# Kernel tuning notes

Hardware: AMD Instinct MI355X
Metric: run time of the kernel (lower is better)

Reference implementation:

```python
import jax, jax.numpy as jnp
import numpy as np

N_NODES = 50000
N_EDGES = 800000
D_FEAT = 128
HIDDEN = 128
BERT_DIM = 768
BATCH = 4096
MAX_ENT = 20
COMB = BERT_DIM + HIDDEN  # 896


def setup_inputs() -> dict:
    key = jax.random.key(0)
    ks = jax.random.split(key, 12)
    article_bert_embeddings = jax.random.normal(ks[0], (BATCH, BERT_DIM), dtype=jnp.float32)
    x = jax.random.normal(ks[1], (N_NODES, D_FEAT), dtype=jnp.float32)
    edge_index = jax.random.randint(ks[2], (2, N_EDGES), 0, N_NODES, dtype=jnp.int64)
    entity_map = jax.random.randint(ks[3], (BATCH, MAX_ENT), 0, N_NODES, dtype=jnp.int64)
    pad = jax.random.uniform(ks[4], (BATCH, MAX_ENT)) < 0.3
    entity_map = jnp.where(pad, jnp.int64(-1), entity_map)
    s = 1.0 / np.sqrt(D_FEAT)
    W1 = jax.random.normal(ks[5], (D_FEAT, HIDDEN), dtype=jnp.float32) * s
    b1 = jnp.zeros((HIDDEN,), dtype=jnp.float32)
    W2 = jax.random.normal(ks[6], (HIDDEN, HIDDEN), dtype=jnp.float32) * (1.0 / np.sqrt(HIDDEN))
    b2 = jnp.zeros((HIDDEN,), dtype=jnp.float32)
    fc1_w = jax.random.normal(ks[7], (COMB, COMB // 2), dtype=jnp.float32) * (1.0 / np.sqrt(COMB))
    fc1_b = jnp.zeros((COMB // 2,), dtype=jnp.float32)
    fc2_w = jax.random.normal(ks[8], (COMB // 2, 1), dtype=jnp.float32) * (1.0 / np.sqrt(COMB // 2))
    fc2_b = jnp.zeros((1,), dtype=jnp.float32)
    return dict(article_bert_embeddings=article_bert_embeddings, x=x,
                edge_index=edge_index, entity_map=entity_map,
                W1=W1, b1=b1, W2=W2, b2=b2,
                fc1_w=fc1_w, fc1_b=fc1_b, fc2_w=fc2_w, fc2_b=fc2_b)


def _gcn_norm(edge_index, n_nodes):
    # add self loops (PyG GCNConv default) and compute symmetric normalization
    loops = jnp.arange(n_nodes, dtype=edge_index.dtype)
    src = jnp.concatenate([edge_index[0], loops])
    dst = jnp.concatenate([edge_index[1], loops])
    deg = jax.ops.segment_sum(jnp.ones_like(dst, dtype=jnp.float32), dst, num_segments=n_nodes)
    dinv = jnp.where(deg > 0, jax.lax.rsqrt(deg), 0.0)
    norm = dinv[src] * dinv[dst]  # [E+N]
    return src, dst, norm


def _gcn_conv(h, W, b, src, dst, norm, n_nodes):
    h = h @ W                                   # [N, H] transform first (cheaper)
    msg = h[src] * norm[:, None]                # [E+N, H] gather
    out = jax.ops.segment_sum(msg, dst, num_segments=n_nodes)
    return out + b


def reference(article_bert_embeddings, x, edge_index, entity_map,
              W1, b1, W2, b2, fc1_w, fc1_b, fc2_w, fc2_b):
    n = x.shape[0]
    src, dst, norm = _gcn_norm(edge_index, n)
    # GNN (dropout in eval mode = identity)
    h = jax.nn.relu(_gcn_conv(x, W1, b1, src, dst, norm, n))
    h = jax.nn.relu(_gcn_conv(h, W2, b2, src, dst, norm, n))
    # ragged mean over entity lists (-1 = padding), fully vectorized
    mask = entity_map >= 0                           # [B, M]
    safe_ids = jnp.where(mask, entity_map, 0)
    gathered = h[safe_ids] * mask[..., None]         # [B, M, H]
    cnt = jnp.maximum(mask.sum(axis=1, keepdims=True).astype(h.dtype), 1.0)
    batch_gnn = gathered.sum(axis=1) / cnt           # [B, H]; rows w/ no entities stay 0
    combined = jnp.concatenate([article_bert_embeddings, batch_gnn], axis=1)
    z = jax.nn.relu(combined @ fc1_w + fc1_b)
    logits = z @ fc2_w + fc2_b
    return jax.nn.sigmoid(logits)
```

## Files before the change

### kernel.cpp

```cpp
#include <hip/hip_runtime.h>
#include <math.h>

typedef __bf16 bf16_t;
typedef __bf16 bfrag8 __attribute__((ext_vector_type(8)));
typedef float  facc4  __attribute__((ext_vector_type(4)));
typedef float  f32x2  __attribute__((ext_vector_type(2)));

#define NBUCK 512
#define BCAP  4096

__device__ inline unsigned short f2b(float x) {
    unsigned int u = __float_as_uint(x);
    unsigned int r = (u + 0x7fffu + ((u >> 16) & 1u)) >> 16;
    return (unsigned short)r;
}
__device__ inline unsigned int pack2(float lo, float hi) {
    return (unsigned int)f2b(lo) | ((unsigned int)f2b(hi) << 16);
}
__device__ inline float blo(unsigned int q) { return __uint_as_float(q << 16); }
__device__ inline float bhi(unsigned int q) { return __uint_as_float(q & 0xffff0000u); }

#if __has_builtin(__builtin_amdgcn_cvt_pk_f32_fp8) && __has_builtin(__builtin_amdgcn_cvt_pk_fp8_f32)
#define HW_FP8 1
#endif

__device__ inline f32x2 fp8pair_dec(unsigned short v) {
#ifdef HW_FP8
    return __builtin_amdgcn_cvt_pk_f32_fp8((int)(unsigned int)v, false);
#else
    f32x2 r;
    unsigned char b0 = (unsigned char)(v & 0xff), b1 = (unsigned char)(v >> 8);
    {
        int e = (b0 >> 3) & 0xf, m = b0 & 7;
        float mag = e ? ldexpf(8.f + m, e - 10) : ldexpf((float)m, -9);
        r.x = (b0 & 0x80) ? -mag : mag;
    }
    {
        int e = (b1 >> 3) & 0xf, m = b1 & 7;
        float mag = e ? ldexpf(8.f + m, e - 10) : ldexpf((float)m, -9);
        r.y = (b1 & 0x80) ? -mag : mag;
    }
    return r;
#endif
}
__device__ inline unsigned char fp8_enc(float x) {
#ifdef HW_FP8
    return (unsigned char)(__builtin_amdgcn_cvt_pk_fp8_f32(x, x, 0, false) & 0xff);
#else
    unsigned char s = (x < 0.f) ? 0x80 : 0;
    float ax = fabsf(x);
    if (!(ax > 0.f)) return s;
    if (ax >= 448.f) return s | 0x7e;
    if (ax < 0.015625f) {
        int q = (int)rintf(ax * 512.f);
        return s | (unsigned char)q;
    }
    int e; float m = frexpf(ax, &e);
    int q = (int)rintf(m * 16.f);
    int E = e - 1;
    if (q == 16) { q = 8; ++E; }
    if (E > 8) return s | 0x7e;
    return s | (unsigned char)(((E + 7) << 3) | (q - 8));
#endif
}

__device__ inline int bucket_of(int d, int N) {
    return (int)(((long long)d * NBUCK) / N);
}

__global__ __launch_bounds__(256) void k_bin2(const int* __restrict__ src,
                                              const int* __restrict__ dst,
                                              int* __restrict__ bcnt,
                                              unsigned int* __restrict__ ebuf,
                                              int E, int N) {
    __shared__ unsigned int sorted[4096];
    __shared__ int hist[NBUCK];
    __shared__ int lstart[NBUCK];
    __shared__ int gbase[NBUCK];
    __shared__ int sm[256];
    int tid = threadIdx.x;
    int base = blockIdx.x * 4096;
    int cnt = min(4096, E - base);
    hist[tid] = 0; hist[tid + 256] = 0;
    __syncthreads();
    unsigned int mye[16]; int myb[16];
#pragma unroll
    for (int i = 0; i < 16; ++i) {
        int idx = i * 256 + tid;
        myb[i] = -1;
        if (idx < cnt) {
            int e = base + idx;
            int s = src[e], d = dst[e];
            mye[i] = ((unsigned int)s << 16) | (unsigned int)d;
            int b = bucket_of(d, N);
            myb[i] = b;
            atomicAdd(&hist[b], 1);
        }
    }
    __syncthreads();
    int p0 = hist[2 * tid], p1 = hist[2 * tid + 1];
    sm[tid] = p0 + p1;
    __syncthreads();
    for (int off = 1; off < 256; off <<= 1) {
        int x = (tid >= off) ? sm[tid - off] : 0;
        __syncthreads();
        sm[tid] += x;
        __syncthreads();
    }
    int excl = sm[tid] - (p0 + p1);
    lstart[2 * tid] = excl;
    lstart[2 * tid + 1] = excl + p0;
    __syncthreads();
    hist[tid] = lstart[tid]; hist[tid + 256] = lstart[tid + 256];
    __syncthreads();
#pragma unroll
    for (int i = 0; i < 16; ++i) {
        if (myb[i] >= 0) {
            int pos = atomicAdd(&hist[myb[i]], 1);
            sorted[pos] = mye[i];
        }
    }
    __syncthreads();
    for (int b = tid; b < NBUCK; b += 256) {
        int c = hist[b] - lstart[b];
        gbase[b] = (c > 0) ? atomicAdd(&bcnt[b], c) : 0;
    }
    __syncthreads();
    for (int idx = tid; idx < cnt; idx += 256) {
        unsigned int v = sorted[idx];
        int b = bucket_of((int)(v & 0xffffu), N);
        ebuf[(size_t)b * BCAP + gbase[b] + (idx - lstart[b])] = v;
    }
}

__global__ __launch_bounds__(256) void k_build2(const unsigned int* __restrict__ ebuf,
                                                const int* __restrict__ bcnt,
                                                int* __restrict__ offs,
                                                float* __restrict__ dinv,
                                                unsigned short* __restrict__ csr,
                                                int N, int E) {
    __shared__ unsigned short seg[BCAP];
    __shared__ int cnt_l[128];
    __shared__ int scan_l[128];
    __shared__ int curs[128];
    __shared__ int smr[256];
    int b = blockIdx.x, tid = threadIdx.x;
    int part = 0;
    for (int j = tid; j < b; j += 256) part += bcnt[j];
    smr[tid] = part;
    __syncthreads();
    for (int off = 128; off > 0; off >>= 1) {
        if (tid < off) smr[tid] += smr[tid + off];
        __syncthreads();
    }
    int base = smr[0];
    int lo = (int)(((long long)b * N + NBUCK - 1) / NBUCK);
    int cnt = bcnt[b];
    int nrange = (int)(((long long)(b + 1) * N + NBUCK - 1) / NBUCK) - lo;
    if (b == 0 && tid == 0) offs[N] = E;
    if (tid < 128) cnt_l[tid] = 0;
    __syncthreads();
    for (int i = tid; i < cnt; i += 256) {
        unsigned int v = ebuf[(size_t)b * BCAP + i];
        atomicAdd(&cnt_l[(int)(v & 0xffffu) - lo], 1);
    }
    __syncthreads();
    if (tid < 128) scan_l[tid] = cnt_l[tid];
    __syncthreads();
    for (int off = 1; off < 128; off <<= 1) {
        int x = 0;
        if (tid < 128 && tid >= off) x = scan_l[tid - off];
        __syncthreads();
        if (tid < 128) scan_l[tid] += x;
        __syncthreads();
    }
    if (tid < 128) {
        int excl = scan_l[tid] - cnt_l[tid];
        curs[tid] = excl;
        if (tid < nrange) {
            offs[lo + tid] = base + excl;
            dinv[lo + tid] = rsqrtf((float)(cnt_l[tid] + 1));
        }
    }
    __syncthreads();
    for (int i = tid; i < cnt; i += 256) {
        unsigned int v = ebuf[(size_t)b * BCAP + i];
        int d = (int)(v & 0xffffu) - lo;
        int p = atomicAdd(&curs[d], 1);
        seg[p] = (unsigned short)(v >> 16);
    }
    __syncthreads();
    for (int i = tid; i < cnt; i += 256) csr[base + i] = seg[i];
}

__global__ __launch_bounds__(256) void k_prep(const float* __restrict__ bert,
                                              unsigned int* __restrict__ bertb, int n8,
                                              const float* __restrict__ W1,
                                              unsigned short* __restrict__ w1t,
                                              const float* __restrict__ W2,
                                              unsigned short* __restrict__ w2t,
                                              const float* __restrict__ Wf,
                                              unsigned short* __restrict__ fwt,
                                              int* __restrict__ bcnt,
                                              float* __restrict__ logacc) {
    __shared__ float tile[64][65];
    int ncvt = (n8 + 255) / 256;
    int bb = blockIdx.x, tid = threadIdx.x;
    if (bb < ncvt) {
        int i = bb * 256 + tid;
        if (i >= n8) return;
        const float4* p = (const float4*)bert + (size_t)i * 2;
        float4 a = p[0], b = p[1];
        uint4 o;
        o.x = pack2(a.x, a.y);
        o.y = pack2(a.z, a.w);
        o.z = pack2(b.x, b.y);
        o.w = pack2(b.z, b.w);
        ((uint4*)bertb)[i] = o;
        return;
    }
    bb -= ncvt;
    if (bb < 128) {
        int i = bb * 256 + tid;
        const float* W = (i < 16384) ? W1 : W2;
        unsigned short* Wt = (i < 16384) ? w1t : w2t;
        int idx = i & 16383;
        int n = idx >> 7, k = idx & 127;
        Wt[idx] = f2b(W[k * 128 + n]);
        return;
    }
    bb -= 128;
    if (bb < 98) {
        int n0 = (bb % 7) * 64, k0 = (bb / 7) * 64;
#pragma unroll
        for (int i = 0; i < 16; ++i) {
            int idx = i * 256 + tid;
            int r = idx >> 6, c = idx & 63;
            tile[r][c] = Wf[(size_t)(k0 + r) * 448 + n0 + c];
        }
        __syncthreads();
#pragma unroll
        for (int i = 0; i < 16; ++i) {
            int idx = i * 256 + tid;
            int c = idx >> 6, r = idx & 63;
            fwt[(size_t)(n0 + c) * 896 + k0 + r] = f2b(tile[r][c]);
        }
        return;
    }
    if (tid < 256) { bcnt[tid] = 0; bcnt[tid + 256] = 0; }
#pragma unroll
    for (int i = 0; i < 16; ++i) logacc[i * 256 + tid] = 0.f;
}

__global__ __launch_bounds__(256) void k_gemm_f32a(const float* __restrict__ A,
                                                   const bf16_t* __restrict__ Bt,
                                                   const float* __restrict__ rs,
                                                   unsigned char* __restrict__ out8, int M) {
    __shared__ bf16_t As[64 * 136];
    __shared__ bf16_t Bs[128 * 136];
    int t = threadIdx.x;
    int wave = t >> 6, lane = t & 63, quad = lane >> 4, l16 = lane & 15;
    int r0 = blockIdx.x * 64;
#pragma unroll
    for (int i = 0; i < 4; ++i) {
        int chunk = t + i * 256;
        int row = chunk >> 4, c8 = (chunk & 15) << 3;
        int gr = r0 + row;
        float4 a0 = make_float4(0.f, 0.f, 0.f, 0.f), a1 = a0;
        if (gr < M) {
            a0 = *(const float4*)&A[(size_t)gr * 128 + c8];
            a1 = *(const float4*)&A[(size_t)gr * 128 + c8 + 4];
        }
        *(uint4*)&As[row * 136 + c8] =
            make_uint4(pack2(a0.x, a0.y), pack2(a0.z, a0.w),
                       pack2(a1.x, a1.y), pack2(a1.z, a1.w));
    }
#pragma unroll
    for (int i = 0; i < 8; ++i) {
        int chunk = t + i * 256;
        int row = chunk >> 4, c8 = (chunk & 15) << 3;
        *(uint4*)&Bs[row * 136 + c8] = *(const uint4*)&Bt[row * 128 + c8];
    }
    __syncthreads();

    facc4 acc[8];
#pragma unroll
    for (int nt = 0; nt < 8; ++nt) acc[nt] = (facc4){0.f, 0.f, 0.f, 0.f};
    int arow = (wave << 4) + l16;
#pragma unroll
    for (int ks = 0; ks < 4; ++ks) {
        int kk = ks * 32 + quad * 8;
        bfrag8 af = *(const bfrag8*)&As[arow * 136 + kk];
#pragma unroll
        for (int nt = 0; nt < 8; ++nt) {
            bfrag8 bf = *(const bfrag8*)&Bs[(nt * 16 + l16) * 136 + kk];
            acc[nt] = __builtin_amdgcn_mfma_f32_16x16x32_bf16(af, bf, acc[nt], 0, 0, 0);
        }
    }
    __syncthreads();
    unsigned char* f8t = (unsigned char*)As;
    int wrow0 = (wave << 4) + quad * 4;
#pragma unroll
    for (int r = 0; r < 4; ++r) {
        int row = wrow0 + r;
        float sc = rs[min(r0 + row, M - 1)];
#pragma unroll
        for (int nt = 0; nt < 8; ++nt)
            f8t[row * 128 + nt * 16 + l16] = fp8_enc(acc[nt][r] * sc);
    }
    __syncthreads();
#pragma unroll
    for (int i = 0; i < 2; ++i) {
        int idx = t + i * 256;
        int row = idx >> 3, cc = (idx & 7) << 4;
        int gr = r0 + row;
        if (gr < M) *(uint4*)&out8[(size_t)gr * 128 + cc] = *(const uint4*)&f8t[row * 128 + cc];
    }
}

__global__ __launch_bounds__(256) void k_gemm_nn128(const bf16_t* __restrict__ A,
                                                    const bf16_t* __restrict__ Bt,
                                                    const float* __restrict__ rs,
                                                    unsigned char* __restrict__ out8, int M) {
    __shared__ bf16_t As[64 * 136];
    __shared__ bf16_t Bs[128 * 136];
    int t = threadIdx.x;
    int wave = t >> 6, lane = t & 63, quad = lane >> 4, l16 = lane & 15;
    int r0 = blockIdx.x * 64;
#pragma unroll
    for (int i = 0; i < 4; ++i) {
        int chunk = t + i * 256;
        int row = chunk >> 4, c8 = (chunk & 15) << 3;
        int gr = r0 + row;
        uint4 v = make_uint4(0u, 0u, 0u, 0u);
        if (gr < M) v = *(const uint4*)&A[(size_t)gr * 128 + c8];
        *(uint4*)&As[row * 136 + c8] = v;
    }
#pragma unroll
    for (int i = 0; i < 8; ++i) {
        int chunk = t + i * 256;
        int row = chunk >> 4, c8 = (chunk & 15) << 3;
        *(uint4*)&Bs[row * 136 + c8] = *(const uint4*)&Bt[row * 128 + c8];
    }
    __syncthreads();

    facc4 acc[8];
#pragma unroll
    for (int nt = 0; nt < 8; ++nt) acc[nt] = (facc4){0.f, 0.f, 0.f, 0.f};
    int arow = (wave << 4) + l16;
#pragma unroll
    for (int ks = 0; ks < 4; ++ks) {
        int kk = ks * 32 + quad * 8;
        bfrag8 af = *(const bfrag8*)&As[arow * 136 + kk];
#pragma unroll
        for (int nt = 0; nt < 8; ++nt) {
            bfrag8 bf = *(const bfrag8*)&Bs[(nt * 16 + l16) * 136 + kk];
            acc[nt] = __builtin_amdgcn_mfma_f32_16x16x32_bf16(af, bf, acc[nt], 0, 0, 0);
        }
    }
    __syncthreads();
    unsigned char* f8t = (unsigned char*)As;
    int wrow0 = (wave << 4) + quad * 4;
#pragma unroll
    for (int r = 0; r < 4; ++r) {
        int row = wrow0 + r;
        float sc = rs[min(r0 + row, M - 1)];
#pragma unroll
        for (int nt = 0; nt < 8; ++nt)
            f8t[row * 128 + nt * 16 + l16] = fp8_enc(acc[nt][r] * sc);
    }
    __syncthreads();
#pragma unroll
    for (int i = 0; i < 2; ++i) {
        int idx = t + i * 256;
        int row = idx >> 3, cc = (idx & 7) << 4;
        int gr = r0 + row;
        if (gr < M) *(uint4*)&out8[(size_t)gr * 128 + cc] = *(const uint4*)&f8t[row * 128 + cc];
    }
}

__global__ __launch_bounds__(256) void k_agg_b(const unsigned short* __restrict__ hx8,
                                               const unsigned short* __restrict__ csr,
                                               const int* __restrict__ offs,
                                               const float* __restrict__ dinv,
                                               const float* __restrict__ bias,
                                               unsigned int* __restrict__ out, int N) {
    int node = blockIdx.x * 4 + (threadIdx.x >> 6);
    int lane = threadIdx.x & 63;
    if (node >= N) return;
    float di = dinv[node];
    f32x2 sf = fp8pair_dec(hx8[(size_t)node * 64 + lane]);
    float acc0 = sf.x, acc1 = sf.y;
    int s0 = offs[node], s1 = offs[node + 1];
    for (int base = s0; base < s1; base += 64) {
        int nloc = min(64, s1 - base);
        int en = 0;
        if (lane < nloc) en = (int)csr[base + lane];
        int j = 0;
        for (; j + 16 <= nloc; j += 16) {
            int sid[16]; unsigned short g[16];
#pragma unroll
            for (int u = 0; u < 16; ++u) sid[u] = __shfl(en, j + u, 64);
#pragma unroll
            for (int u = 0; u < 16; ++u) g[u] = hx8[(size_t)sid[u] * 64 + lane];
#pragma unroll
            for (int u = 0; u < 16; ++u) { f32x2 d = fp8pair_dec(g[u]); acc0 += d.x; acc1 += d.y; }
        }
        for (; j + 4 <= nloc; j += 4) {
            int sid[4]; unsigned short g[4];
#pragma unroll
            for (int u = 0; u < 4; ++u) sid[u] = __shfl(en, j + u, 64);
#pragma unroll
            for (int u = 0; u < 4; ++u) g[u] = hx8[(size_t)sid[u] * 64 + lane];
#pragma unroll
            for (int u = 0; u < 4; ++u) { f32x2 d = fp8pair_dec(g[u]); acc0 += d.x; acc1 += d.y; }
        }
        for (; j < nloc; ++j) {
            int srcn = __shfl(en, j, 64);
            f32x2 d = fp8pair_dec(hx8[(size_t)srcn * 64 + lane]);
            acc0 += d.x; acc1 += d.y;
        }
    }
    float2 bb = *(const float2*)&bias[lane * 2];
    float v0 = fmaxf(acc0 * di + bb.x, 0.f);
    float v1 = fmaxf(acc1 * di + bb.y, 0.f);
    out[(size_t)node * 64 + lane] = pack2(v0, v1);
}

__global__ __launch_bounds__(256) void k_pool_b(const unsigned int* __restrict__ h,
                                                const int* __restrict__ ent,
                                                unsigned int* __restrict__ out) {
    int r = blockIdx.x * 4 + (threadIdx.x >> 6);
    int lane = threadIdx.x & 63;
    float a0 = 0.f, a1 = 0.f;
    int cnt = 0;
#pragma unroll
    for (int m = 0; m < 20; ++m) {
        int id = ent[r * 20 + m];
        if (id >= 0) {
            unsigned int q = h[(size_t)id * 64 + lane];
            a0 += blo(q); a1 += bhi(q); cnt++;
        }
    }
    float inv = 1.f / (float)max(cnt, 1);
    out[(size_t)r * 64 + lane] = pack2(a0 * inv, a1 * inv);
}

__global__ __launch_bounds__(256) void k_mlp1_mfma(const bf16_t* __restrict__ bertb,
                                                   const bf16_t* __restrict__ gnnb,
                                                   const bf16_t* __restrict__ fwt,
                                                   const float* __restrict__ fb,
                                                   const float* __restrict__ w2,
                                                   float* __restrict__ logacc) {
    __shared__ bf16_t As[64 * 136];
    __shared__ bf16_t Bs[64 * 136];
    int t = threadIdx.x;
    int wave = t >> 6, lane = t & 63, quad = lane >> 4, l16 = lane & 15;
    int r0 = blockIdx.x * 64, c0 = blockIdx.y * 64;
    facc4 acc[4];
#pragma unroll
    for (int nt = 0; nt < 4; ++nt) acc[nt] = (facc4){0.f, 0.f, 0.f, 0.f};

    for (int ks = 0; ks < 7; ++ks) {
#pragma unroll
        for (int i = 0; i < 4; ++i) {
            int chunk = t + i * 256;
            int row = chunk >> 4, c8 = (chunk & 15) << 3;
            int gr = r0 + row;
            const bf16_t* srcp = (ks < 6) ? &bertb[(size_t)gr * 768 + ks * 128 + c8]
                                          : &gnnb[(size_t)gr * 128 + c8];
            *(uint4*)&As[row * 136 + c8] = *(const uint4*)srcp;
        }
#pragma unroll
        for (int i = 0; i < 4; ++i) {
            int chunk = t + i * 256;
            int row = chunk >> 4, c8 = (chunk & 15) << 3;
            *(uint4*)&Bs[row * 136 + c8] =
                *(const uint4*)&fwt[(size_t)(c0 + row) * 896 + ks * 128 + c8];
        }
        __syncthreads();
        int arow = (wave << 4) + l16;
#pragma unroll
        for (int sub = 0; sub < 4; ++sub) {
            int kk = sub * 32 + quad * 8;
            bfrag8 af = *(const bfrag8*)&As[arow * 136 + kk];
#pragma unroll
            for (int nt = 0; nt < 4; ++nt) {
                bfrag8 bf = *(const bfrag8*)&Bs[(nt * 16 + l16) * 136 + kk];
                acc[nt] = __builtin_amdgcn_mfma_f32_16x16x32_bf16(af, bf, acc[nt], 0, 0, 0);
            }
        }
        __syncthreads();
    }
    int rbase = r0 + (wave << 4) + quad * 4;
    float part[4] = {0.f, 0.f, 0.f, 0.f};
#pragma unroll
    for (int nt = 0; nt < 4; ++nt) {
        int col = c0 + nt * 16 + l16;
        float bb = fb[col];
        float ww = w2[col];
#pragma unroll
        for (int r = 0; r < 4; ++r)
            part[r] += fmaxf(acc[nt][r] + bb, 0.f) * ww;
    }
#pragma unroll
    for (int m = 8; m >= 1; m >>= 1) {
#pragma unroll
        for (int r = 0; r < 4; ++r) part[r] += __shfl_xor(part[r], m, 64);
    }
    if (l16 == 0) {
#pragma unroll
        for (int r = 0; r < 4; ++r) atomicAdd(&logacc[rbase + r], part[r]);
    }
}

__global__ void k_sig(const float* __restrict__ logacc, const float* __restrict__ b,
                      float* __restrict__ out, int B) {
    int i = blockIdx.x * 256 + threadIdx.x;
    if (i < B) out[i] = 1.f / (1.f + expf(-(logacc[i] + b[0])));
}

extern "C" void kernel_launch(void* const* d_in, const int* in_sizes, int n_in,
                              void* d_out, int out_size, void* d_ws, size_t ws_size,
                              hipStream_t stream) {
    const float* bert = (const float*)d_in[0];
    const float* x    = (const float*)d_in[1];
    const int*   ei   = (const int*)d_in[2];
    const int*   ent  = (const int*)d_in[3];
    const float* W1   = (const float*)d_in[4];
    const float* b1   = (const float*)d_in[5];
    const float* W2   = (const float*)d_in[6];
    const float* b2   = (const float*)d_in[7];
    const float* fc1w = (const float*)d_in[8];
    const float* fc1b = (const float*)d_in[9];
    const float* fc2w = (const float*)d_in[10];
    const float* fc2b = (const float*)d_in[11];
    float* out = (float*)d_out;

    const int N = in_sizes[1] / 128;
    const int E = in_sizes[2] / 2;
    const int B = in_sizes[0] / 768;

    const int* srcv = ei;
    const int* dstv = ei + E;

    char* wsp = (char*)d_ws;
    size_t off = 0;
    auto alloc = [&](size_t bytes) -> void* {
        void* p = wsp + off;
        off += (bytes + 255) & ~(size_t)255;
        return p;
    };
    float* dinv   = (float*)alloc((size_t)N * 4);
    int*   offs   = (int*)alloc((size_t)(N + 1) * 4);
    int*   bcnt   = (int*)alloc(NBUCK * 4);
    float* logacc = (float*)alloc((size_t)B * 4);
    unsigned int*   ebuf  = (unsigned int*)alloc((size_t)NBUCK * BCAP * 4);
    unsigned short* csr16 = (unsigned short*)alloc((size_t)E * 2);
    bf16_t* bertb = (bf16_t*)alloc((size_t)B * 768 * 2);
    bf16_t* w1t   = (bf16_t*)alloc(128 * 128 * 2);
    bf16_t* w2t   = (bf16_t*)alloc(128 * 128 * 2);
    bf16_t* fwt   = (bf16_t*)alloc((size_t)896 * 448 * 2);
    unsigned char* g8buf = (unsigned char*)alloc((size_t)N * 128);
    bf16_t* hbuf  = (bf16_t*)alloc((size_t)N * 128 * 2);
    bf16_t* gnnb  = (bf16_t*)alloc((size_t)B * 128 * 2);
    (void)ws_size; (void)n_in; (void)out_size;

    int nb8 = B * 768 / 8;
    int ncvt = (nb8 + 255) / 256;
    int nprep = ncvt + 128 + 98 + 1;
    k_prep<<<nprep, 256, 0, stream>>>(bert, (unsigned int*)bertb, nb8,
                                      W1, (unsigned short*)w1t, W2, (unsigned short*)w2t,
                                      fc1w, (unsigned short*)fwt, bcnt, logacc);
    k_bin2  <<<(E + 4095) / 4096, 256, 0, stream>>>(srcv, dstv, bcnt, ebuf, E, N);
    k_build2<<<NBUCK, 256, 0, stream>>>(ebuf, bcnt, offs, dinv, csr16, N, E);

    int gb = (N + 63) / 64;
    k_gemm_f32a<<<gb, 256, 0, stream>>>(x, w1t, dinv, g8buf, N);
    k_agg_b<<<(N + 3) / 4, 256, 0, stream>>>((const unsigned short*)g8buf, csr16, offs, dinv, b1,
                                             (unsigned int*)hbuf, N);
    k_gemm_nn128<<<gb, 256, 0, stream>>>(hbuf, w2t, dinv, g8buf, N);
    k_agg_b<<<(N + 3) / 4, 256, 0, stream>>>((const unsigned short*)g8buf, csr16, offs, dinv, b2,
                                             (unsigned int*)hbuf, N);
    k_pool_b<<<B / 4, 256, 0, stream>>>((const unsigned int*)hbuf, ent, (unsigned int*)gnnb);
    k_mlp1_mfma<<<dim3(B / 64, 7), 256, 0, stream>>>(bertb, gnnb, fwt, fc1b, fc2w, logacc);
    k_sig<<<(B + 255) / 256, 256, 0, stream>>>(logacc, fc2b, out, B);
}
```

Measured before the change: 217.6 us.

## Fuse layer-1 aggregation into layer-2 GEMM, merge prep/bin, fold sigmoid into MLP

Layer-1 neighbor aggregation (fp8 gather, bias, ReLU) now runs inside the layer-2 GEMM kernel, writing rows straight into shared memory instead of a bf16 hbuf round trip. The prep and edge-binning kernels become one launch, and buffer zeroing moves to a memset. The final sigmoid runs in the last-finishing MLP block, found with an atomic done counter, which removes a launch. Cost: the fused aggregation kernel has only N/64 blocks with 4 waves each doing 16 rows serially, so there is less parallelism for the latency-bound gather than in the old N/4-block aggregation.

```diff
diff --git a/kernel.cpp b/kernel.cpp
--- a/kernel.cpp
+++ b/kernel.cpp
@@ -68,68 +68,124 @@
     return (int)(((long long)d * NBUCK) / N);
 }
 
-__global__ __launch_bounds__(256) void k_bin2(const int* __restrict__ src,
-                                              const int* __restrict__ dst,
-                                              int* __restrict__ bcnt,
-                                              unsigned int* __restrict__ ebuf,
-                                              int E, int N) {
-    __shared__ unsigned int sorted[4096];
-    __shared__ int hist[NBUCK];
-    __shared__ int lstart[NBUCK];
-    __shared__ int gbase[NBUCK];
-    __shared__ int sm[256];
-    int tid = threadIdx.x;
-    int base = blockIdx.x * 4096;
-    int cnt = min(4096, E - base);
-    hist[tid] = 0; hist[tid + 256] = 0;
-    __syncthreads();
-    unsigned int mye[16]; int myb[16];
-#pragma unroll
-    for (int i = 0; i < 16; ++i) {
-        int idx = i * 256 + tid;
-        myb[i] = -1;
-        if (idx < cnt) {
-            int e = base + idx;
-            int s = src[e], d = dst[e];
-            mye[i] = ((unsigned int)s << 16) | (unsigned int)d;
-            int b = bucket_of(d, N);
-            myb[i] = b;
-            atomicAdd(&hist[b], 1);
-        }
-    }
-    __syncthreads();
-    int p0 = hist[2 * tid], p1 = hist[2 * tid + 1];
-    sm[tid] = p0 + p1;
-    __syncthreads();
-    for (int off = 1; off < 256; off <<= 1) {
-        int x = (tid >= off) ? sm[tid - off] : 0;
-        __syncthreads();
-        sm[tid] += x;
-        __syncthreads();
-    }
-    int excl = sm[tid] - (p0 + p1);
-    lstart[2 * tid] = excl;
-    lstart[2 * tid + 1] = excl + p0;
-    __syncthreads();
-    hist[tid] = lstart[tid]; hist[tid + 256] = lstart[tid + 256];
-    __syncthreads();
-#pragma unroll
-    for (int i = 0; i < 16; ++i) {
-        if (myb[i] >= 0) {
-            int pos = atomicAdd(&hist[myb[i]], 1);
-            sorted[pos] = mye[i];
-        }
-    }
-    __syncthreads();
-    for (int b = tid; b < NBUCK; b += 256) {
-        int c = hist[b] - lstart[b];
-        gbase[b] = (c > 0) ? atomicAdd(&bcnt[b], c) : 0;
-    }
-    __syncthreads();
-    for (int idx = tid; idx < cnt; idx += 256) {
-        unsigned int v = sorted[idx];
-        int b = bucket_of((int)(v & 0xffffu), N);
-        ebuf[(size_t)b * BCAP + gbase[b] + (idx - lstart[b])] = v;
+__global__ __launch_bounds__(256) void k_prepbin(const int* __restrict__ src,
+                                                 const int* __restrict__ dst,
+                                                 int* __restrict__ bcnt,
+                                                 unsigned int* __restrict__ ebuf,
+                                                 int E, int N,
+                                                 const float* __restrict__ bert,
+                                                 unsigned int* __restrict__ bertb, int n8,
+                                                 const float* __restrict__ W1,
+                                                 unsigned short* __restrict__ w1t,
+                                                 const float* __restrict__ W2,
+                                                 unsigned short* __restrict__ w2t,
+                                                 const float* __restrict__ Wf,
+                                                 unsigned short* __restrict__ fwt) {
+    __shared__ __align__(16) unsigned char smem[23552];
+    int bb = blockIdx.x, tid = threadIdx.x;
+    int nbin = (E + 4095) / 4096;
+    if (bb < nbin) {
+        unsigned int* sorted = (unsigned int*)smem;
+        int* hist   = (int*)(smem + 16384);
+        int* lstart = (int*)(smem + 18432);
+        int* gbase  = (int*)(smem + 20480);
+        int* sm     = (int*)(smem + 22528);
+        int base = bb * 4096;
+        int cnt = min(4096, E - base);
+        hist[tid] = 0; hist[tid + 256] = 0;
+        __syncthreads();
+        unsigned int mye[16]; int myb[16];
+#pragma unroll
+        for (int i = 0; i < 16; ++i) {
+            int idx = i * 256 + tid;
+            myb[i] = -1;
+            if (idx < cnt) {
+                int e = base + idx;
+                int s = src[e], d = dst[e];
+                mye[i] = ((unsigned int)s << 16) | (unsigned int)d;
+                int b = bucket_of(d, N);
+                myb[i] = b;
+                atomicAdd(&hist[b], 1);
+            }
+        }
+        __syncthreads();
+        int p0 = hist[2 * tid], p1 = hist[2 * tid + 1];
+        sm[tid] = p0 + p1;
+        __syncthreads();
+        for (int off = 1; off < 256; off <<= 1) {
+            int x = (tid >= off) ? sm[tid - off] : 0;
+            __syncthreads();
+            sm[tid] += x;
+            __syncthreads();
+        }
+        int excl = sm[tid] - (p0 + p1);
+        lstart[2 * tid] = excl;
+        lstart[2 * tid + 1] = excl + p0;
+        __syncthreads();
+        hist[tid] = lstart[tid]; hist[tid + 256] = lstart[tid + 256];
+        __syncthreads();
+#pragma unroll
+        for (int i = 0; i < 16; ++i) {
+            if (myb[i] >= 0) {
+                int pos = atomicAdd(&hist[myb[i]], 1);
+                sorted[pos] = mye[i];
+            }
+        }
+        __syncthreads();
+        for (int b = tid; b < NBUCK; b += 256) {
+            int c = hist[b] - lstart[b];
+            gbase[b] = (c > 0) ? atomicAdd(&bcnt[b], c) : 0;
+        }
+        __syncthreads();
+        for (int idx = tid; idx < cnt; idx += 256) {
+            unsigned int v = sorted[idx];
+            int b = bucket_of((int)(v & 0xffffu), N);
+            ebuf[(size_t)b * BCAP + gbase[b] + (idx - lstart[b])] = v;
+        }
+        return;
+    }
+    bb -= nbin;
+    int ncvt = (n8 + 255) / 256;
+    if (bb < ncvt) {
+        int i = bb * 256 + tid;
+        if (i >= n8) return;
+        const float4* p = (const float4*)bert + (size_t)i * 2;
+        float4 a = p[0], b = p[1];
+        uint4 o;
+        o.x = pack2(a.x, a.y);
+        o.y = pack2(a.z, a.w);
+        o.z = pack2(b.x, b.y);
+        o.w = pack2(b.z, b.w);
+        ((uint4*)bertb)[i] = o;
+        return;
+    }
+    bb -= ncvt;
+    if (bb < 128) {
+        int i = bb * 256 + tid;
+        const float* W = (i < 16384) ? W1 : W2;
+        unsigned short* Wt = (i < 16384) ? w1t : w2t;
+        int idx = i & 16383;
+        int n = idx >> 7, k = idx & 127;
+        Wt[idx] = f2b(W[k * 128 + n]);
+        return;
+    }
+    bb -= 128;
+    {
+        float* tile = (float*)smem;
+        int n0 = (bb % 7) * 64, k0 = (bb / 7) * 64;
+#pragma unroll
+        for (int i = 0; i < 16; ++i) {
+            int idx = i * 256 + tid;
+            int r = idx >> 6, c = idx & 63;
+            tile[r * 65 + c] = Wf[(size_t)(k0 + r) * 448 + n0 + c];
+        }
+        __syncthreads();
+#pragma unroll
+        for (int i = 0; i < 16; ++i) {
+            int idx = i * 256 + tid;
+            int c = idx >> 6, r = idx & 63;
+            fwt[(size_t)(n0 + c) * 896 + k0 + r] = f2b(tile[r * 65 + c]);
+        }
     }
 }
 
@@ -193,65 +249,6 @@
     for (int i = tid; i < cnt; i += 256) csr[base + i] = seg[i];
 }
 
-__global__ __launch_bounds__(256) void k_prep(const float* __restrict__ bert,
-                                              unsigned int* __restrict__ bertb, int n8,
-                                              const float* __restrict__ W1,
-                                              unsigned short* __restrict__ w1t,
-                                              const float* __restrict__ W2,
-                                              unsigned short* __restrict__ w2t,
-                                              const float* __restrict__ Wf,
-                                              unsigned short* __restrict__ fwt,
-                                              int* __restrict__ bcnt,
-                                              float* __restrict__ logacc) {
-    __shared__ float tile[64][65];
-    int ncvt = (n8 + 255) / 256;
-    int bb = blockIdx.x, tid = threadIdx.x;
-    if (bb < ncvt) {
-        int i = bb * 256 + tid;
-        if (i >= n8) return;
-        const float4* p = (const float4*)bert + (size_t)i * 2;
-        float4 a = p[0], b = p[1];
-        uint4 o;
-        o.x = pack2(a.x, a.y);
-        o.y = pack2(a.z, a.w);
-        o.z = pack2(b.x, b.y);
-        o.w = pack2(b.z, b.w);
-        ((uint4*)bertb)[i] = o;
-        return;
-    }
-    bb -= ncvt;
-    if (bb < 128) {
-        int i = bb * 256 + tid;
-        const float* W = (i < 16384) ? W1 : W2;
-        unsigned short* Wt = (i < 16384) ? w1t : w2t;
-        int idx = i & 16383;
-        int n = idx >> 7, k = idx & 127;
-        Wt[idx] = f2b(W[k * 128 + n]);
-        return;
-    }
-    bb -= 128;
-    if (bb < 98) {
-        int n0 = (bb % 7) * 64, k0 = (bb / 7) * 64;
-#pragma unroll
-        for (int i = 0; i < 16; ++i) {
-            int idx = i * 256 + tid;
-            int r = idx >> 6, c = idx & 63;
-            tile[r][c] = Wf[(size_t)(k0 + r) * 448 + n0 + c];
-        }
-        __syncthreads();
-#pragma unroll
-        for (int i = 0; i < 16; ++i) {
-            int idx = i * 256 + tid;
-            int c = idx >> 6, r = idx & 63;
-            fwt[(size_t)(n0 + c) * 896 + k0 + r] = f2b(tile[r][c]);
-        }
-        return;
-    }
-    if (tid < 256) { bcnt[tid] = 0; bcnt[tid + 256] = 0; }
-#pragma unroll
-    for (int i = 0; i < 16; ++i) logacc[i * 256 + tid] = 0.f;
-}
-
 __global__ __launch_bounds__(256) void k_gemm_f32a(const float* __restrict__ A,
                                                    const bf16_t* __restrict__ Bt,
                                                    const float* __restrict__ rs,
@@ -318,30 +315,69 @@
     }
 }
 
-__global__ __launch_bounds__(256) void k_gemm_nn128(const bf16_t* __restrict__ A,
-                                                    const bf16_t* __restrict__ Bt,
-                                                    const float* __restrict__ rs,
-                                                    unsigned char* __restrict__ out8, int M) {
+__global__ __launch_bounds__(256) void k_fag(const unsigned short* __restrict__ hx8,
+                                             const unsigned short* __restrict__ csr,
+                                             const int* __restrict__ offs,
+                                             const float* __restrict__ dinv,
+                                             const float* __restrict__ bias,
+                                             const bf16_t* __restrict__ Bt,
+                                             unsigned char* __restrict__ out8,
+                                             int M) {
     __shared__ bf16_t As[64 * 136];
     __shared__ bf16_t Bs[128 * 136];
     int t = threadIdx.x;
     int wave = t >> 6, lane = t & 63, quad = lane >> 4, l16 = lane & 15;
     int r0 = blockIdx.x * 64;
 #pragma unroll
-    for (int i = 0; i < 4; ++i) {
-        int chunk = t + i * 256;
-        int row = chunk >> 4, c8 = (chunk & 15) << 3;
-        int gr = r0 + row;
-        uint4 v = make_uint4(0u, 0u, 0u, 0u);
-        if (gr < M) v = *(const uint4*)&A[(size_t)gr * 128 + c8];
-        *(uint4*)&As[row * 136 + c8] = v;
-    }
-#pragma unroll
     for (int i = 0; i < 8; ++i) {
         int chunk = t + i * 256;
         int row = chunk >> 4, c8 = (chunk & 15) << 3;
         *(uint4*)&Bs[row * 136 + c8] = *(const uint4*)&Bt[row * 128 + c8];
     }
+    float2 bb = *(const float2*)&bias[lane * 2];
+    for (int rr = 0; rr < 16; ++rr) {
+        int lrow = (wave << 4) + rr;
+        int row = r0 + lrow;
+        float v0 = 0.f, v1 = 0.f;
+        if (row < M) {
+            float di = dinv[row];
+            f32x2 sf = fp8pair_dec(hx8[(size_t)row * 64 + lane]);
+            float acc0 = sf.x, acc1 = sf.y;
+            int s0 = offs[row], s1 = offs[row + 1];
+            for (int base = s0; base < s1; base += 64) {
+                int nloc = min(64, s1 - base);
+                int en = 0;
+                if (lane < nloc) en = (int)csr[base + lane];
+                int j = 0;
+                for (; j + 16 <= nloc; j += 16) {
+                    int sid[16]; unsigned short g[16];
+#pragma unroll
+                    for (int u = 0; u < 16; ++u) sid[u] = __shfl(en, j + u, 64);
+#pragma unroll
+                    for (int u = 0; u < 16; ++u) g[u] = hx8[(size_t)sid[u] * 64 + lane];
+#pragma unroll
+                    for (int u = 0; u < 16; ++u) { f32x2 d = fp8pair_dec(g[u]); acc0 += d.x; acc1 += d.y; }
+                }
+                for (; j + 4 <= nloc; j += 4) {
+                    int sid[4]; unsigned short g[4];
+#pragma unroll
+                    for (int u = 0; u < 4; ++u) sid[u] = __shfl(en, j + u, 64);
+#pragma unroll
+                    for (int u = 0; u < 4; ++u) g[u] = hx8[(size_t)sid[u] * 64 + lane];
+#pragma unroll
+                    for (int u = 0; u < 4; ++u) { f32x2 d = fp8pair_dec(g[u]); acc0 += d.x; acc1 += d.y; }
+                }
+                for (; j < nloc; ++j) {
+                    int srcn = __shfl(en, j, 64);
+                    f32x2 d = fp8pair_dec(hx8[(size_t)srcn * 64 + lane]);
+                    acc0 += d.x; acc1 += d.y;
+                }
+            }
+            v0 = fmaxf(acc0 * di + bb.x, 0.f);
+            v1 = fmaxf(acc1 * di + bb.y, 0.f);
+        }
+        *(unsigned int*)&As[lrow * 136 + 2 * lane] = pack2(v0, v1);
+    }
     __syncthreads();
 
     facc4 acc[8];
@@ -364,7 +400,7 @@
 #pragma unroll
     for (int r = 0; r < 4; ++r) {
         int row = wrow0 + r;
-        float sc = rs[min(r0 + row, M - 1)];
+        float sc = dinv[min(r0 + row, M - 1)];
 #pragma unroll
         for (int nt = 0; nt < 8; ++nt)
             f8t[row * 128 + nt * 16 + l16] = fp8_enc(acc[nt][r] * sc);
@@ -451,9 +487,13 @@
                                                    const bf16_t* __restrict__ fwt,
                                                    const float* __restrict__ fb,
                                                    const float* __restrict__ w2,
-                                                   float* __restrict__ logacc) {
+                                                   float* __restrict__ logacc,
+                                                   int* __restrict__ donecnt,
+                                                   const float* __restrict__ b2,
+                                                   float* __restrict__ outp, int B) {
     __shared__ bf16_t As[64 * 136];
     __shared__ bf16_t Bs[64 * 136];
+    __shared__ int lastflag;
     int t = threadIdx.x;
     int wave = t >> 6, lane = t & 63, quad = lane >> 4, l16 = lane & 15;
     int r0 = blockIdx.x * 64, c0 = blockIdx.y * 64;
@@ -512,12 +552,21 @@
 #pragma unroll
         for (int r = 0; r < 4; ++r) atomicAdd(&logacc[rbase + r], part[r]);
     }
-}
-
-__global__ void k_sig(const float* __restrict__ logacc, const float* __restrict__ b,
-                      float* __restrict__ out, int B) {
-    int i = blockIdx.x * 256 + threadIdx.x;
-    if (i < B) out[i] = 1.f / (1.f + expf(-(logacc[i] + b[0])));
+    __threadfence();
+    __syncthreads();
+    if (t == 0) {
+        int done = atomicAdd(donecnt, 1);
+        lastflag = (done == (int)(gridDim.x * gridDim.y) - 1);
+    }
+    __syncthreads();
+    if (lastflag) {
+        __threadfence();
+        float bias2 = b2[0];
+        for (int i = t; i < B; i += 256) {
+            float v = atomicAdd(&logacc[i], 0.0f);
+            outp[i] = 1.f / (1.f + expf(-(v + bias2)));
+        }
+    }
 }
 
 extern "C" void kernel_launch(void* const* d_in, const int* in_sizes, int n_in,
@@ -551,38 +600,41 @@
         off += (bytes + 255) & ~(size_t)255;
         return p;
     };
+    int*   bcnt   = (int*)alloc(NBUCK * 4);
+    float* logacc = (float*)alloc((size_t)B * 4);
+    int*   donecnt= (int*)alloc(4);
     float* dinv   = (float*)alloc((size_t)N * 4);
     int*   offs   = (int*)alloc((size_t)(N + 1) * 4);
-    int*   bcnt   = (int*)alloc(NBUCK * 4);
-    float* logacc = (float*)alloc((size_t)B * 4);
     unsigned int*   ebuf  = (unsigned int*)alloc((size_t)NBUCK * BCAP * 4);
     unsigned short* csr16 = (unsigned short*)alloc((size_t)E * 2);
     bf16_t* bertb = (bf16_t*)alloc((size_t)B * 768 * 2);
     bf16_t* w1t   = (bf16_t*)alloc(128 * 128 * 2);
     bf16_t* w2t   = (bf16_t*)alloc(128 * 128 * 2);
     bf16_t* fwt   = (bf16_t*)alloc((size_t)896 * 448 * 2);
-    unsigned char* g8buf = (unsigned char*)alloc((size_t)N * 128);
+    unsigned char* g8a = (unsigned char*)alloc((size_t)N * 128);
+    unsigned char* g8b = (unsigned char*)alloc((size_t)N * 128);
     bf16_t* hbuf  = (bf16_t*)alloc((size_t)N * 128 * 2);
     bf16_t* gnnb  = (bf16_t*)alloc((size_t)B * 128 * 2);
     (void)ws_size; (void)n_in; (void)out_size;
 
+    hipMemsetAsync(bcnt, 0, 2048 + 16384 + 256, stream);
+
     int nb8 = B * 768 / 8;
-    int ncvt = (nb8 + 255) / 256;
-    int nprep = ncvt + 128 + 98 + 1;
-    k_prep<<<nprep, 256, 0, stream>>>(bert, (unsigned int*)bertb, nb8,
-                                      W1, (unsigned short*)w1t, W2, (unsigned short*)w2t,
-                                      fc1w, (unsigned short*)fwt, bcnt, logacc);
-    k_bin2  <<<(E + 4095) / 4096, 256, 0, stream>>>(srcv, dstv, bcnt, ebuf, E, N);
+    int nbin = (E + 4095) / 4096;
+    int nprep = nbin + (nb8 + 255) / 256 + 128 + 98;
+    k_prepbin<<<nprep, 256, 0, stream>>>(srcv, dstv, bcnt, ebuf, E, N,
+                                         bert, (unsigned int*)bertb, nb8,
+                                         W1, (unsigned short*)w1t, W2, (unsigned short*)w2t,
+                                         fc1w, (unsigned short*)fwt);
     k_build2<<<NBUCK, 256, 0, stream>>>(ebuf, bcnt, offs, dinv, csr16, N, E);
 
     int gb = (N + 63) / 64;
-    k_gemm_f32a<<<gb, 256, 0, stream>>>(x, w1t, dinv, g8buf, N);
-    k_agg_b<<<(N + 3) / 4, 256, 0, stream>>>((const unsigned short*)g8buf, csr16, offs, dinv, b1,
-                                             (unsigned int*)hbuf, N);
-    k_gemm_nn128<<<gb, 256, 0, stream>>>(hbuf, w2t, dinv, g8buf, N);
-    k_agg_b<<<(N + 3) / 4, 256, 0, stream>>>((const unsigned short*)g8buf, csr16, offs, dinv, b2,
+    k_gemm_f32a<<<gb, 256, 0, stream>>>(x, w1t, dinv, g8a, N);
+    k_fag<<<gb, 256, 0, stream>>>((const unsigned short*)g8a, csr16, offs, dinv, b1,
+                                  w2t, g8b, N);
+    k_agg_b<<<(N + 3) / 4, 256, 0, stream>>>((const unsigned short*)g8b, csr16, offs, dinv, b2,
                                              (unsigned int*)hbuf, N);
     k_pool_b<<<B / 4, 256, 0, stream>>>((const unsigned int*)hbuf, ent, (unsigned int*)gnnb);
-    k_mlp1_mfma<<<dim3(B / 64, 7), 256, 0, stream>>>(bertb, gnnb, fwt, fc1b, fc2w, logacc);
-    k_sig<<<(B + 255) / 256, 256, 0, stream>>>(logacc, fc2b, out, B);
-}
+    k_mlp1_mfma<<<dim3(B / 64, 7), 256, 0, stream>>>(bertb, gnnb, fwt, fc1b, fc2w,
+                                                     logacc, donecnt, fc2b, out, B);
+}
```

Measured after the change: 278.9 us. +28.2%, slower.
